# Optimization experiments

Measured on AMD Instinct MI355X. Metric: run time of the kernel, lower is better.

## Reference

```python
import jax, jax.numpy as jnp
import numpy as np

N = 50000
NEG_SLOPE = 0.01  # F.leaky_relu default


def gcn_conv(x, edge_index, edge_weight, W, b):
    """PyG GCNConv: h = x @ W; symmetric-normalized aggregation with self-loops; + bias."""
    n = x.shape[0]
    h = x @ W                                # [N, out]
    src, dst = edge_index[0], edge_index[1]
    # degree includes self-loop weight 1.0 per node
    deg = jax.ops.segment_sum(edge_weight, dst, num_segments=n) + 1.0
    dinv = jax.lax.rsqrt(deg)                # deg >= 1, no zero guard needed
    norm = dinv[src] * edge_weight * dinv[dst]
    agg = jax.ops.segment_sum(norm[:, None] * h[src], dst, num_segments=n)
    agg = agg + (dinv * dinv)[:, None] * h   # self-loop contribution: deg^-1 * h_i
    return agg + b


def setup_inputs() -> dict:
    key = jax.random.key(0)
    ks = jax.random.split(key, 24)
    in_size, hid, out = 256, 64, 32
    E = 800000
    d = {}
    for i, nm in enumerate(["x1", "x2", "x3"]):
        d[nm] = jax.random.normal(ks[i], (N, in_size), dtype=jnp.float32)
    for i, nm in enumerate(["edge_index1", "edge_index2", "edge_index3"]):
        d[nm] = jax.random.randint(ks[3 + i], (2, E), 0, N, dtype=jnp.int32)
    for i, nm in enumerate(["edge_weight1", "edge_weight2", "edge_weight3"]):
        d[nm] = jax.random.uniform(ks[6 + i], (E,), dtype=jnp.float32)
    s_in = 1.0 / np.sqrt(in_size)
    s_h = 1.0 / np.sqrt(hid)
    for i, nm in enumerate(["W1", "W2", "W3"]):
        d[nm] = jax.random.uniform(ks[9 + i], (in_size, hid), minval=-s_in, maxval=s_in, dtype=jnp.float32)
    for i, nm in enumerate(["b1", "b2", "b3"]):
        d[nm] = jax.random.uniform(ks[12 + i], (hid,), minval=-s_in, maxval=s_in, dtype=jnp.float32)
    d["fc_w"] = jax.random.uniform(ks[15], (hid, 1), minval=-s_h, maxval=s_h, dtype=jnp.float32)
    d["fc_b"] = jax.random.uniform(ks[16], (1,), minval=-s_h, maxval=s_h, dtype=jnp.float32)
    for i, nm in enumerate(["W11", "W22", "W33"]):
        d[nm] = jax.random.uniform(ks[17 + i], (hid, out), minval=-s_h, maxval=s_h, dtype=jnp.float32)
    for i, nm in enumerate(["b11", "b22", "b33"]):
        d[nm] = jax.random.uniform(ks[20 + i], (out,), minval=-s_h, maxval=s_h, dtype=jnp.float32)
    return d


def reference(x1, x2, x3, edge_index1, edge_index2, edge_index3,
              edge_weight1, edge_weight2, edge_weight3,
              W1, W2, W3, b1, b2, b3, fc_w, fc_b,
              W11, W22, W33, b11, b22, b33):
    # branch embeddings (dropout is identity in eval mode)
    e1 = jax.nn.relu(gcn_conv(x1, edge_index1, edge_weight1, W1, b1))
    e2 = jax.nn.relu(gcn_conv(x2, edge_index2, edge_weight2, W2, b2))
    e3 = jax.nn.relu(gcn_conv(x3, edge_index3, edge_weight3, W3, b3))
    # attention coefficients
    c1 = jnp.exp(jax.nn.leaky_relu(e1 @ fc_w + fc_b, NEG_SLOPE))  # [N,1]
    c2 = jnp.exp(jax.nn.leaky_relu(e2 @ fc_w + fc_b, NEG_SLOPE))
    c3 = jnp.exp(jax.nn.leaky_relu(e3 @ fc_w + fc_b, NEG_SLOPE))
    cd = c1 + c2 + c3
    coef1, coef2, coef3 = c1 / cd, c2 / cd, c3 / cd
    combined = e1 * coef1 + e2 * coef2 + e3 * coef3
    out1 = gcn_conv(combined, edge_index1, edge_weight1, W11, b11)
    out2 = gcn_conv(combined, edge_index2, edge_weight2, W22, b22)
    out3 = gcn_conv(combined, edge_index3, edge_weight3, W33, b33)
    return (out1 + out2 + out3, coef1, coef2, coef3)
```

## Files before the change

kernel.cpp:

```cpp
#include <hip/hip_runtime.h>
#include <hip/hip_fp16.h>
#include <math.h>

#define NN    50000
#define INF_  256
#define HID   64
#define OUTF  32
#define EE    800000
#define TOTN  (3 * NN)
#define NBKT  196
#define NBIN  (3 * NBKT)
#define CBLK  196
#define NCNT  (3 * CBLK)
#define GB    782
#define NGEMM (3 * GB)
#define MAXB  5120
#define NBLK  12500

typedef unsigned long long u64;
typedef unsigned int       u32;
typedef unsigned short     u16;
typedef unsigned char      u8;
typedef _Float16           f16;
typedef f16   f16x8 __attribute__((ext_vector_type(8)));
typedef f16   f16x4 __attribute__((ext_vector_type(4)));
typedef float f32x4 __attribute__((ext_vector_type(4)));

__global__ __launch_bounds__(256) void k_prep(
        const float* __restrict__ W1, const float* __restrict__ W2, const float* __restrict__ W3,
        f16* __restrict__ Wt2, u32* __restrict__ bin_total) {
    int blk = blockIdx.x, t = threadIdx.x;
    if (blk == 3) {
        for (int i = t; i < NBIN; i += 256) bin_total[i] = 0;
        return;
    }
    const float* W = (blk == 0) ? W1 : (blk == 1) ? W2 : W3;
    f16* wt = Wt2 + blk * 16384;
    for (int idx = t; idx < 16384; idx += 256) {
        int e    = idx & 7;
        int lane = (idx >> 3) & 63;
        int kt   = (idx >> 9) & 7;
        int c    = idx >> 12;
        int col  = c * 16 + (lane & 15);
        int k    = kt * 32 + ((lane >> 4) << 3) + e;
        wt[idx] = (f16)W[k * HID + col];
    }
}

__global__ __launch_bounds__(256) void k_count(
        const int* __restrict__ ei1, const int* __restrict__ ei2, const int* __restrict__ ei3,
        u32* __restrict__ bin_total, u32* __restrict__ blockbase) {
    __shared__ u32 bins[NBKT];
    int cb  = blockIdx.x;
    int br  = cb / CBLK;
    int blk = cb - br * CBLK;
    const int* ei = (br == 0) ? ei1 : (br == 1) ? ei2 : ei3;
    int t = threadIdx.x;
    for (int i = t; i < NBKT; i += 256) bins[i] = 0;
    __syncthreads();
    int e0 = blk * 4096;
#pragma unroll
    for (int k = 0; k < 16; ++k) {
        int e = e0 + k * 256 + t;
        if (e < EE) atomicAdd(&bins[(u32)ei[EE + e] >> 8], 1u);
    }
    __syncthreads();
    for (int i = t; i < NBKT; i += 256) {
        u32 c = bins[i];
        u32 base = atomicAdd(&bin_total[br * NBKT + i], c);
        blockbase[cb * NBKT + i] = base;
    }
}

__global__ __launch_bounds__(256) void k_scan(const u32* __restrict__ bin_total,
                                              u32* __restrict__ binstart) {
    __shared__ u32 s[256];
    int t = threadIdx.x;
    u32 c[3]; u32 sum = 0;
#pragma unroll
    for (int k = 0; k < 3; ++k) {
        int i = t * 3 + k;
        c[k] = (i < NBIN) ? bin_total[i] : 0;
        sum += c[k];
    }
    s[t] = sum;
    __syncthreads();
    for (int d = 1; d < 256; d <<= 1) {
        u32 v = (t >= d) ? s[t - d] : 0;
        __syncthreads();
        s[t] += v;
        __syncthreads();
    }
    u32 run = s[t] - sum;
#pragma unroll
    for (int k = 0; k < 3; ++k) {
        int i = t * 3 + k;
        if (i < NBIN) binstart[i] = run;
        run += c[k];
    }
    if (t == 255) binstart[NBIN] = run;
}

__global__ __launch_bounds__(256) void k_scatgemm(
        const int* __restrict__ ei1, const int* __restrict__ ei2, const int* __restrict__ ei3,
        const float* __restrict__ ew1, const float* __restrict__ ew2, const float* __restrict__ ew3,
        const u32* __restrict__ binstart, const u32* __restrict__ blockbase,
        u64* __restrict__ bucketed,
        const float* __restrict__ x1, const float* __restrict__ x2, const float* __restrict__ x3,
        const f16* __restrict__ Wt2, __half* __restrict__ h) {
    __shared__ __align__(16) char smem[36864];
    int bid = blockIdx.x;
    int q = bid / 5, r = bid - q * 5;
    int t = threadIdx.x;

    if (r == 4) {
        u64* ent  = (u64*)smem;
        u32* acnt = (u32*)(smem + 32768);
        u32* ascn = acnt + 256;
        u32* acur = ascn + 256;
        u32* adel = acur + 256;
        int cb  = q;
        int br  = cb / CBLK;
        int blk = cb - br * CBLK;
        const int*   ei = (br == 0) ? ei1 : (br == 1) ? ei2 : ei3;
        const float* ew = (br == 0) ? ew1 : (br == 1) ? ew2 : ew3;
        acnt[t] = 0; acur[t] = 0;
        __syncthreads();
        int e0 = blk * 4096;
        int tot = EE - e0; if (tot > 4096) tot = 4096;
#pragma unroll
        for (int k = 0; k < 16; ++k) {
            int e = e0 + k * 256 + t;
            if (e < EE) atomicAdd(&acnt[(u32)ei[EE + e] >> 8], 1u);
        }
        __syncthreads();
        ascn[t] = acnt[t];
        __syncthreads();
        for (int d = 1; d < 256; d <<= 1) {
            u32 v = (t >= d) ? ascn[t - d] : 0;
            __syncthreads();
            ascn[t] += v;
            __syncthreads();
        }
        if (t < NBKT)
            adel[t] = binstart[br * NBKT + t] + blockbase[cb * NBKT + t]
                      - (ascn[t] - acnt[t]);
        __syncthreads();
#pragma unroll
        for (int k = 0; k < 16; ++k) {
            int e = e0 + k * 256 + t;
            if (e < EE) {
                u32 dst = (u32)ei[EE + e];
                u32 src = (u32)ei[e];
                u32 bkt = dst >> 8;
                u16 w16 = __half_as_ushort(__float2half(ew[e]));
                u32 rnk = atomicAdd(&acur[bkt], 1u);
                u32 ls  = ascn[bkt] - acnt[bkt] + rnk;
                ent[ls] = ((u64)bkt << 48) | ((u64)w16 << 32)
                        | ((u64)src << 8) | (u64)(dst & 0xffu);
            }
        }
        __syncthreads();
        for (int i = t; i < tot; i += 256) {
            u64 ev = ent[i];
            u32 bkt = (u32)(ev >> 48) & 0xffu;
            bucketed[adel[bkt] + i] = ev;
        }
        return;
    }

    int gid = q * 4 + r;
    if (gid >= NGEMM) return;
    f16 (*xl)[264] = reinterpret_cast<f16(*)[264]>(smem);
    int b = gid / GB;
    int row_base = (gid - b * GB) * 64;
    const float4* x4 = reinterpret_cast<const float4*>((b == 0) ? x1 : (b == 1) ? x2 : x3);
    const f16* wt2 = Wt2 + b * 16384;
    __half* hb = h + (size_t)b * NN * HID;

    float4 v[16];
#pragma unroll
    for (int j = 0; j < 16; ++j) {
        int flat = j * 256 + t;
        int gr = row_base + (flat >> 6);
        v[j] = (gr < NN) ? x4[(size_t)row_base * 64 + flat]
                         : make_float4(0.f, 0.f, 0.f, 0.f);
    }
#pragma unroll
    for (int j = 0; j < 16; ++j) {
        int flat = j * 256 + t;
        int rr = flat >> 6, c4 = flat & 63;
        f16x4 p = {(f16)v[j].x, (f16)v[j].y, (f16)v[j].z, (f16)v[j].w};
        *(f16x4*)&xl[rr][c4 * 4] = p;
    }
    __syncthreads();

    int w    = t >> 6;
    int lane = t & 63;
    int lrow = lane & 15;
    int lk   = (lane >> 4) * 8;
    int arow = (w << 4) + lrow;

    f32x4 acc[4] = {{0,0,0,0},{0,0,0,0},{0,0,0,0},{0,0,0,0}};
#pragma unroll
    for (int kt = 0; kt < 8; ++kt) {
        f16x8 af = *(const f16x8*)&xl[arow][kt * 32 + lk];
#pragma unroll
        for (int c = 0; c < 4; ++c) {
            f16x8 bf = *(const f16x8*)&wt2[((c * 8 + kt) * 64 + lane) * 8];
            acc[c] = __builtin_amdgcn_mfma_f32_16x16x32_f16(af, bf, acc[c], 0, 0, 0);
        }
    }
    int orow0 = row_base + (w << 4) + ((lane >> 4) << 2);
#pragma unroll
    for (int c = 0; c < 4; ++c) {
#pragma unroll
        for (int i = 0; i < 4; ++i) {
            int row = orow0 + i;
            if (row < NN) hb[(size_t)row * HID + c * 16 + lrow] = __float2half(acc[c][i]);
        }
    }
}

__global__ __launch_bounds__(256) void k_bucket(
        const u64* __restrict__ bucketed, const u32* __restrict__ bin_total,
        const u32* __restrict__ binstart,
        u32* __restrict__ nodeinfo, float* __restrict__ dinv,
        u32* __restrict__ csr, __half* __restrict__ h) {
    __shared__ u32   scnt[256];
    __shared__ float swsum[256];
    __shared__ u32   scur[256];
    __shared__ u32   sscan[256];
    __shared__ float sdiv[256];
    __shared__ u32   lcsr[MAXB];
    int bin = blockIdx.x;
    int br  = bin / NBKT;
    int bkt = bin - br * NBKT;
    int t = threadIdx.x;
    u32 base = binstart[bin];
    u32 ecnt = bin_total[bin];
    scnt[t] = 0; swsum[t] = 0.f; scur[t] = 0;
    __syncthreads();
    for (u32 i = t; i < ecnt; i += 256) {
        u64 e = bucketed[base + i];
        u32 dl = (u32)e & 0xffu;
        atomicAdd(&scnt[dl], 1u);
        atomicAdd(&swsum[dl], __half2float(__ushort_as_half((u16)((e >> 32) & 0xffffu))));
    }
    __syncthreads();
    sscan[t] = scnt[t];
    __syncthreads();
    for (int d = 1; d < 256; d <<= 1) {
        u32 v = (t >= d) ? sscan[t - d] : 0;
        __syncthreads();
        sscan[t] += v;
        __syncthreads();
    }
    u32 lstart = sscan[t] - scnt[t];
    float d = rsqrtf(1.0f + swsum[t]);
    sdiv[t] = d;
    int n = bkt * 256 + t;
    if (n < NN) {
        int gi = br * NN + n;
        nodeinfo[gi] = ((base + lstart) << 10) | scnt[t];
        dinv[gi]     = d;
    }
    __syncthreads();
    for (u32 i = t; i < ecnt; i += 256) {
        u64 e = bucketed[base + i];
        u32 dl  = (u32)e & 0xffu;
        u32 src = (u32)(e >> 8) & 0xffffu;
        u32 w16 = (u32)(e >> 32) & 0xffffu;
        u32 rnk = atomicAdd(&scur[dl], 1u);
        u32 ls  = sscan[dl] - scnt[dl];
        lcsr[ls + rnk] = (w16 << 16) | src;
    }
    __syncthreads();
    for (u32 i = t; i < ecnt; i += 256) csr[base + i] = lcsr[i];

    int nrows = NN - bkt * 256; if (nrows > 256) nrows = 256;
    u32* hrow = (u32*)(h + ((size_t)br * NN + (size_t)bkt * 256) * HID);
    for (int i = t; i < nrows * 32; i += 256) {
        float dd = sdiv[i >> 5];
        __half2 hv = *(__half2*)&hrow[i];
        float2 v = __half22float2(hv);
        __half2 rr = __float22half2_rn(make_float2(v.x * dd, v.y * dd));
        hrow[i] = *(u32*)&rr;
    }
}

__global__ __launch_bounds__(256) void k_agg1(
        const u32* __restrict__ csr, const u32* __restrict__ nodeinfo,
        const float* __restrict__ dinv,
        const float* __restrict__ b1, const float* __restrict__ b2, const float* __restrict__ b3,
        const __half* __restrict__ h, __half* __restrict__ e) {
    int bid = blockIdx.x;
    int br  = bid / NBLK;
    int nb  = bid - br * NBLK;
    int t   = threadIdx.x;
    int f2  = t & 31;
    int eo  = (t >> 5) & 1;
    int sub = __builtin_amdgcn_readfirstlane(t >> 6);
    int n   = nb * 4 + sub;

    const float* bi = (br == 0) ? b1 : (br == 1) ? b2 : b3;
    const __half2* hb2 = (const __half2*)(h + (size_t)br * NN * HID);
    int i   = br * NN + n;
    u32 inf = nodeinfo[i];
    int cc  = (int)(inf & 1023u);
    int st  = (int)(inf >> 10);
    float d = dinv[i];
    float2 hs = __half22float2(hb2[(size_t)n * 32 + f2]);

    float ax = 0.f, ay = 0.f;
    int cm1 = cc - 1;
    for (int j = 0; j < cc; j += 16) {
        u32 ee[8]; __half2 vv[8];
#pragma unroll
        for (int u = 0; u < 8; ++u) {
            int jj = j + 2 * u + eo;
            ee[u] = csr[st + (jj < cm1 ? jj : cm1)];
            if (jj >= cc) ee[u] &= 0xffffu;
        }
#pragma unroll
        for (int u = 0; u < 8; ++u)
            vv[u] = hb2[(size_t)(ee[u] & 0xffff) * 32 + f2];
#pragma unroll
        for (int u = 0; u < 8; ++u) {
            float w = __half2float(__ushort_as_half((u16)(ee[u] >> 16)));
            float2 v = __half22float2(vv[u]);
            ax = fmaf(w, v.x, ax);
            ay = fmaf(w, v.y, ay);
        }
    }
    ax += __shfl_xor(ax, 32);
    ay += __shfl_xor(ay, 32);
    float2 bv = ((const float2*)bi)[f2];
    float ex = fmaxf(bv.x + d * (hs.x + ax), 0.f);
    float ey = fmaxf(bv.y + d * (hs.y + ay), 0.f);
    if (eo == 0)
        ((__half2*)e)[((size_t)br * NN + n) * 32 + f2] = __float22half2_rn(make_float2(ex, ey));
}

__global__ __launch_bounds__(256) void k_attn(
        const __half* __restrict__ e,
        const float* __restrict__ fc_w, const float* __restrict__ fc_b,
        __half* __restrict__ comb, float* __restrict__ coef_out) {
    int t    = threadIdx.x;
    int lane = t & 63;
    int sub  = __builtin_amdgcn_readfirstlane(t >> 6);
    int half = lane >> 5;
    int f2   = lane & 31;
    int n    = blockIdx.x * 8 + sub * 2 + half;
    float2 wv = ((const float2*)fc_w)[f2];
    float fb = fc_b[0];
    const __half2* e2 = (const __half2*)e;

    float2 ev[3]; float c[3];
#pragma unroll
    for (int b = 0; b < 3; ++b) {
        ev[b] = __half22float2(e2[((size_t)b * NN + n) * 32 + f2]);
        float dd = ev[b].x * wv.x + ev[b].y * wv.y;
#pragma unroll
        for (int off = 16; off > 0; off >>= 1) dd += __shfl_xor(dd, off);
        float z = dd + fb;
        z = (z > 0.f) ? z : 0.01f * z;
        c[b] = expf(z);
    }
    float cd = c[0] + c[1] + c[2];
    float coef0 = c[0] / cd, coef1 = c[1] / cd, coef2 = c[2] / cd;
    float cx = ev[0].x * coef0 + ev[1].x * coef1 + ev[2].x * coef2;
    float cy = ev[0].y * coef0 + ev[1].y * coef1 + ev[2].y * coef2;
    ((__half2*)comb)[(size_t)n * 32 + f2] = __float22half2_rn(make_float2(cx, cy));
    if (f2 == 0) {
        coef_out[n]          = coef0;
        coef_out[NN + n]     = coef1;
        coef_out[2 * NN + n] = coef2;
    }
}

__global__ __launch_bounds__(256) void k_gemm2(
        const __half* __restrict__ comb,
        const float* __restrict__ W11, const float* __restrict__ W22, const float* __restrict__ W33,
        const float* __restrict__ dinv, __half* __restrict__ h2) {
    __shared__ float Wls[3][HID][OUTF];
    __shared__ __half cl[8][HID];
    int t = threadIdx.x;
    {
        const float4* w40 = reinterpret_cast<const float4*>(W11);
        const float4* w41 = reinterpret_cast<const float4*>(W22);
        const float4* w42 = reinterpret_cast<const float4*>(W33);
        float4* d0 = reinterpret_cast<float4*>(&Wls[0][0][0]);
        float4* d1 = reinterpret_cast<float4*>(&Wls[1][0][0]);
        float4* d2 = reinterpret_cast<float4*>(&Wls[2][0][0]);
#pragma unroll
        for (int j = 0; j < 2; ++j) {
            d0[t + j * 256] = w40[t + j * 256];
            d1[t + j * 256] = w41[t + j * 256];
            d2[t + j * 256] = w42[t + j * 256];
        }
    }
    int row0 = blockIdx.x * 8;
    ((u32*)cl)[t] = ((const u32*)(comb + (size_t)row0 * HID))[t];
    __syncthreads();

    int col = t & 31;
    int rr  = t >> 5;
    int row = row0 + rr;
    float a0 = 0.f, a1 = 0.f, a2 = 0.f;
    for (int k = 0; k < HID; ++k) {
        float cv = __half2float(cl[rr][k]);
        a0 = fmaf(cv, Wls[0][k][col], a0);
        a1 = fmaf(cv, Wls[1][k][col], a1);
        a2 = fmaf(cv, Wls[2][k][col], a2);
    }
    float d0 = dinv[row], d1 = dinv[NN + row], d2 = dinv[2 * NN + row];
    h2[(size_t)0 * NN * OUTF + (size_t)row * OUTF + col] = __float2half(a0 * d0);
    h2[(size_t)1 * NN * OUTF + (size_t)row * OUTF + col] = __float2half(a1 * d1);
    h2[(size_t)2 * NN * OUTF + (size_t)row * OUTF + col] = __float2half(a2 * d2);
}

__global__ __launch_bounds__(256) void k_agg2p(
        const u32* __restrict__ csr, const u32* __restrict__ nodeinfo,
        const float* __restrict__ dinv,
        const __half* __restrict__ h2, float* __restrict__ outp) {
    int bid = blockIdx.x;
    int br  = bid / NBLK;
    int nb  = bid - br * NBLK;
    int t   = threadIdx.x;
    int f2  = t & 15;
    int eo  = (t >> 4) & 3;
    int sub = __builtin_amdgcn_readfirstlane(t >> 6);
    int n   = nb * 4 + sub;

    int i   = br * NN + n;
    u32 inf = nodeinfo[i];
    int cc  = (int)(inf & 1023u);
    int st  = (int)(inf >> 10);
    const __half2* h2b = (const __half2*)(h2 + (size_t)br * NN * OUTF);
    float ax = 0.f, ay = 0.f;
    int cm1 = cc - 1;
    for (int j = 0; j < cc; j += 16) {
        u32 ee[4]; __half2 vv[4];
#pragma unroll
        for (int u = 0; u < 4; ++u) {
            int jj = j + 4 * u + eo;
            ee[u] = csr[st + (jj < cm1 ? jj : cm1)];
            if (jj >= cc) ee[u] &= 0xffffu;
        }
#pragma unroll
        for (int u = 0; u < 4; ++u)
            vv[u] = h2b[(size_t)(ee[u] & 0xffff) * 16 + f2];
#pragma unroll
        for (int u = 0; u < 4; ++u) {
            float w = __half2float(__ushort_as_half((u16)(ee[u] >> 16)));
            float2 v = __half22float2(vv[u]);
            ax = fmaf(w, v.x, ax);
            ay = fmaf(w, v.y, ay);
        }
    }
    ax += __shfl_xor(ax, 16); ay += __shfl_xor(ay, 16);
    ax += __shfl_xor(ax, 32); ay += __shfl_xor(ay, 32);
    float d = dinv[i];
    float2 hs = __half22float2(h2b[(size_t)n * 16 + f2]);
    if (eo == 0)
        ((float2*)outp)[((size_t)br * NN + n) * 16 + f2] =
            make_float2(d * (ax + hs.x), d * (ay + hs.y));
}

__global__ __launch_bounds__(256) void k_sum(
        const float* __restrict__ outp,
        const float* __restrict__ b11, const float* __restrict__ b22, const float* __restrict__ b33,
        float* __restrict__ out) {
    int i = blockIdx.x * 256 + threadIdx.x;
    int f2 = i & 15;
    const float2* p = (const float2*)outp;
    float2 v0 = p[i];
    float2 v1 = p[(size_t)NN * 16 + i];
    float2 v2 = p[(size_t)2 * NN * 16 + i];
    float2 bA = ((const float2*)b11)[f2];
    float2 bB = ((const float2*)b22)[f2];
    float2 bC = ((const float2*)b33)[f2];
    ((float2*)out)[i] = make_float2(v0.x + v1.x + v2.x + bA.x + bB.x + bC.x,
                                    v0.y + v1.y + v2.y + bA.y + bB.y + bC.y);
}

extern "C" void kernel_launch(void* const* d_in, const int* in_sizes, int n_in,
                              void* d_out, int out_size, void* d_ws, size_t ws_size,
                              hipStream_t stream) {
    const float* x1  = (const float*)d_in[0];
    const float* x2  = (const float*)d_in[1];
    const float* x3  = (const float*)d_in[2];
    const int*   ei1 = (const int*)d_in[3];
    const int*   ei2 = (const int*)d_in[4];
    const int*   ei3 = (const int*)d_in[5];
    const float* ew1 = (const float*)d_in[6];
    const float* ew2 = (const float*)d_in[7];
    const float* ew3 = (const float*)d_in[8];
    const float* W1  = (const float*)d_in[9];
    const float* W2  = (const float*)d_in[10];
    const float* W3  = (const float*)d_in[11];
    const float* b1  = (const float*)d_in[12];
    const float* b2  = (const float*)d_in[13];
    const float* b3  = (const float*)d_in[14];
    const float* fcw = (const float*)d_in[15];
    const float* fcb = (const float*)d_in[16];
    const float* W11 = (const float*)d_in[17];
    const float* W22 = (const float*)d_in[18];
    const float* W33 = (const float*)d_in[19];
    const float* b11 = (const float*)d_in[20];
    const float* b22 = (const float*)d_in[21];
    const float* b33 = (const float*)d_in[22];

    float* out = (float*)d_out;
    float* coef_out = out + (size_t)NN * OUTF;

    u64*   bucketed  = (u64*)d_ws;
    float* outp      = (float*)d_ws;
    u32*   csr       = (u32*)(bucketed + 3 * EE);
    u32*   bin_total = csr + 3 * EE;
    u32*   binstart  = bin_total + NBIN;
    u32*   blockbase = binstart + NBIN + 4;
    float* dinv      = (float*)(blockbase + NCNT * NBKT);
    u32*   nodeinfo  = (u32*)(dinv + TOTN);
    f16*   Wt2       = (f16*)(nodeinfo + TOTN);
    __half* h        = (__half*)(Wt2 + 3 * 16384);
    __half* comb     = h + (size_t)TOTN * HID;
    __half* h2       = comb + (size_t)NN * HID;
    __half* e        = h2 + (size_t)TOTN * OUTF;

    k_prep<<<dim3(4), 256, 0, stream>>>(W1, W2, W3, Wt2, bin_total);
    k_count<<<dim3(NCNT), 256, 0, stream>>>(ei1, ei2, ei3, bin_total, blockbase);
    k_scan<<<dim3(1), 256, 0, stream>>>(bin_total, binstart);
    k_scatgemm<<<dim3(NCNT * 5), 256, 0, stream>>>(ei1, ei2, ei3, ew1, ew2, ew3,
                                                   binstart, blockbase, bucketed,
                                                   x1, x2, x3, Wt2, h);
    k_bucket<<<dim3(NBIN), 256, 0, stream>>>(bucketed, bin_total, binstart,
                                             nodeinfo, dinv, csr, h);

    k_agg1<<<dim3(3 * NBLK), 256, 0, stream>>>(csr, nodeinfo, dinv, b1, b2, b3, h, e);
    k_attn<<<dim3(NN / 8), 256, 0, stream>>>(e, fcw, fcb, comb, coef_out);
    k_gemm2<<<dim3(NN / 8), 256, 0, stream>>>(comb, W11, W22, W33, dinv, h2);
    k_agg2p<<<dim3(3 * NBLK), 256, 0, stream>>>(csr, nodeinfo, dinv, h2, outp);
    k_sum<<<dim3(3125), 256, 0, stream>>>(outp, b11, b22, b33, out);
}
```

Before: 272.5 us.

## Replace count and scan passes with fixed-capacity bins and atomic cursors

Removes the separate edge-count kernel and the single-block scan kernel. Each bucket now gets a fixed slot of MAXB entries in the workspace. Scatter blocks reserve space in a bucket with an atomicAdd on a per-bucket cursor. The scatter blocks also cache destination indices in registers, so the destination array is read once instead of twice. This drops two launches and a full pass over the edge list. In exchange it uses a larger workspace and relies on no bucket holding more than MAXB edges.

```diff
diff --git a/kernel.cpp b/kernel.cpp
--- a/kernel.cpp
+++ b/kernel.cpp
@@ -20,7 +20,6 @@
 typedef unsigned long long u64;
 typedef unsigned int       u32;
 typedef unsigned short     u16;
-typedef unsigned char      u8;
 typedef _Float16           f16;
 typedef f16   f16x8 __attribute__((ext_vector_type(8)));
 typedef f16   f16x4 __attribute__((ext_vector_type(4)));
@@ -28,10 +27,10 @@
 
 __global__ __launch_bounds__(256) void k_prep(
         const float* __restrict__ W1, const float* __restrict__ W2, const float* __restrict__ W3,
-        f16* __restrict__ Wt2, u32* __restrict__ bin_total) {
+        f16* __restrict__ Wt2, u32* __restrict__ bin_cursor) {
     int blk = blockIdx.x, t = threadIdx.x;
     if (blk == 3) {
-        for (int i = t; i < NBIN; i += 256) bin_total[i] = 0;
+        for (int i = t; i < NBIN; i += 256) bin_cursor[i] = 0;
         return;
     }
     const float* W = (blk == 0) ? W1 : (blk == 1) ? W2 : W3;
@@ -47,65 +46,10 @@
     }
 }
 
-__global__ __launch_bounds__(256) void k_count(
-        const int* __restrict__ ei1, const int* __restrict__ ei2, const int* __restrict__ ei3,
-        u32* __restrict__ bin_total, u32* __restrict__ blockbase) {
-    __shared__ u32 bins[NBKT];
-    int cb  = blockIdx.x;
-    int br  = cb / CBLK;
-    int blk = cb - br * CBLK;
-    const int* ei = (br == 0) ? ei1 : (br == 1) ? ei2 : ei3;
-    int t = threadIdx.x;
-    for (int i = t; i < NBKT; i += 256) bins[i] = 0;
-    __syncthreads();
-    int e0 = blk * 4096;
-#pragma unroll
-    for (int k = 0; k < 16; ++k) {
-        int e = e0 + k * 256 + t;
-        if (e < EE) atomicAdd(&bins[(u32)ei[EE + e] >> 8], 1u);
-    }
-    __syncthreads();
-    for (int i = t; i < NBKT; i += 256) {
-        u32 c = bins[i];
-        u32 base = atomicAdd(&bin_total[br * NBKT + i], c);
-        blockbase[cb * NBKT + i] = base;
-    }
-}
-
-__global__ __launch_bounds__(256) void k_scan(const u32* __restrict__ bin_total,
-                                              u32* __restrict__ binstart) {
-    __shared__ u32 s[256];
-    int t = threadIdx.x;
-    u32 c[3]; u32 sum = 0;
-#pragma unroll
-    for (int k = 0; k < 3; ++k) {
-        int i = t * 3 + k;
-        c[k] = (i < NBIN) ? bin_total[i] : 0;
-        sum += c[k];
-    }
-    s[t] = sum;
-    __syncthreads();
-    for (int d = 1; d < 256; d <<= 1) {
-        u32 v = (t >= d) ? s[t - d] : 0;
-        __syncthreads();
-        s[t] += v;
-        __syncthreads();
-    }
-    u32 run = s[t] - sum;
-#pragma unroll
-    for (int k = 0; k < 3; ++k) {
-        int i = t * 3 + k;
-        if (i < NBIN) binstart[i] = run;
-        run += c[k];
-    }
-    if (t == 255) binstart[NBIN] = run;
-}
-
 __global__ __launch_bounds__(256) void k_scatgemm(
         const int* __restrict__ ei1, const int* __restrict__ ei2, const int* __restrict__ ei3,
         const float* __restrict__ ew1, const float* __restrict__ ew2, const float* __restrict__ ew3,
-        const u32* __restrict__ binstart, const u32* __restrict__ blockbase,
-        u64* __restrict__ bucketed,
+        u32* __restrict__ bin_cursor, u64* __restrict__ bucketed,
         const float* __restrict__ x1, const float* __restrict__ x2, const float* __restrict__ x3,
         const f16* __restrict__ Wt2, __half* __restrict__ h) {
     __shared__ __align__(16) char smem[36864];
@@ -128,10 +72,14 @@
         __syncthreads();
         int e0 = blk * 4096;
         int tot = EE - e0; if (tot > 4096) tot = 4096;
+        u32 dstv[16];
 #pragma unroll
         for (int k = 0; k < 16; ++k) {
             int e = e0 + k * 256 + t;
-            if (e < EE) atomicAdd(&acnt[(u32)ei[EE + e] >> 8], 1u);
+            if (e < EE) {
+                dstv[k] = (u32)ei[EE + e];
+                atomicAdd(&acnt[dstv[k] >> 8], 1u);
+            }
         }
         __syncthreads();
         ascn[t] = acnt[t];
@@ -142,15 +90,17 @@
             ascn[t] += v;
             __syncthreads();
         }
-        if (t < NBKT)
-            adel[t] = binstart[br * NBKT + t] + blockbase[cb * NBKT + t]
-                      - (ascn[t] - acnt[t]);
+        if (t < NBKT) {
+            u32 cnt = acnt[t];
+            u32 base = cnt ? atomicAdd(&bin_cursor[br * NBKT + t], cnt) : 0;
+            adel[t] = (u32)(br * NBKT + t) * MAXB + base - (ascn[t] - acnt[t]);
+        }
         __syncthreads();
 #pragma unroll
         for (int k = 0; k < 16; ++k) {
             int e = e0 + k * 256 + t;
             if (e < EE) {
-                u32 dst = (u32)ei[EE + e];
+                u32 dst = dstv[k];
                 u32 src = (u32)ei[e];
                 u32 bkt = dst >> 8;
                 u16 w16 = __half_as_ushort(__float2half(ew[e]));
@@ -223,8 +173,7 @@
 }
 
 __global__ __launch_bounds__(256) void k_bucket(
-        const u64* __restrict__ bucketed, const u32* __restrict__ bin_total,
-        const u32* __restrict__ binstart,
+        const u64* __restrict__ bucketed, const u32* __restrict__ bin_cursor,
         u32* __restrict__ nodeinfo, float* __restrict__ dinv,
         u32* __restrict__ csr, __half* __restrict__ h) {
     __shared__ u32   scnt[256];
@@ -237,8 +186,8 @@
     int br  = bin / NBKT;
     int bkt = bin - br * NBKT;
     int t = threadIdx.x;
-    u32 base = binstart[bin];
-    u32 ecnt = bin_total[bin];
+    u32 base = (u32)bin * MAXB;
+    u32 ecnt = bin_cursor[bin];
     scnt[t] = 0; swsum[t] = 0.f; scur[t] = 0;
     __syncthreads();
     for (u32 i = t; i < ecnt; i += 256) {
@@ -517,11 +466,9 @@
 
     u64*   bucketed  = (u64*)d_ws;
     float* outp      = (float*)d_ws;
-    u32*   csr       = (u32*)(bucketed + 3 * EE);
-    u32*   bin_total = csr + 3 * EE;
-    u32*   binstart  = bin_total + NBIN;
-    u32*   blockbase = binstart + NBIN + 4;
-    float* dinv      = (float*)(blockbase + NCNT * NBKT);
+    u32*   csr       = (u32*)(bucketed + (size_t)NBIN * MAXB);
+    u32*   bin_cursor= csr + (size_t)NBIN * MAXB;
+    float* dinv      = (float*)(bin_cursor + NBIN + 4);
     u32*   nodeinfo  = (u32*)(dinv + TOTN);
     f16*   Wt2       = (f16*)(nodeinfo + TOTN);
     __half* h        = (__half*)(Wt2 + 3 * 16384);
@@ -529,13 +476,11 @@
     __half* h2       = comb + (size_t)NN * HID;
     __half* e        = h2 + (size_t)TOTN * OUTF;
 
-    k_prep<<<dim3(4), 256, 0, stream>>>(W1, W2, W3, Wt2, bin_total);
-    k_count<<<dim3(NCNT), 256, 0, stream>>>(ei1, ei2, ei3, bin_total, blockbase);
-    k_scan<<<dim3(1), 256, 0, stream>>>(bin_total, binstart);
+    k_prep<<<dim3(4), 256, 0, stream>>>(W1, W2, W3, Wt2, bin_cursor);
     k_scatgemm<<<dim3(NCNT * 5), 256, 0, stream>>>(ei1, ei2, ei3, ew1, ew2, ew3,
-                                                   binstart, blockbase, bucketed,
+                                                   bin_cursor, bucketed,
                                                    x1, x2, x3, Wt2, h);
-    k_bucket<<<dim3(NBIN), 256, 0, stream>>>(bucketed, bin_total, binstart,
+    k_bucket<<<dim3(NBIN), 256, 0, stream>>>(bucketed, bin_cursor,
                                              nodeinfo, dinv, csr, h);
 
     k_agg1<<<dim3(3 * NBLK), 256, 0, stream>>>(csr, nodeinfo, dinv, b1, b2, b3, h, e);
```

New measurement: 254.1 us. 1.07x faster.
